# Kernel tuning notes

Measured on AMD Instinct MI355X. Metric: run time of the kernel, lower is better.

## Reference

```python
import jax, jax.numpy as jnp
import numpy as np

B, N, K = 4, 4096, 20
IN_C, OUT_C = 32, 32
EPS = 1e-5


def setup_inputs() -> dict:
    key = jax.random.key(0)
    ks = jax.random.split(key, 10)
    s = 0.05
    return {
        "x": jax.random.normal(ks[0], (B, 3, N), dtype=jnp.float32),
        "feature": jax.random.normal(ks[1], (B, IN_C, N), dtype=jnp.float32),
        "w_mlp": jax.random.normal(ks[2], (IN_C, 7), dtype=jnp.float32) * s,     # Conv1d(7, in_c, 1)
        "b_mlp": jax.random.normal(ks[3], (IN_C,), dtype=jnp.float32) * s,
        "w_att": jax.random.normal(ks[4], (2 * IN_C, 2 * IN_C), dtype=jnp.float32) * s,  # Conv1d(2C,2C,1,bias=False)
        "w_conv": jax.random.normal(ks[5], (OUT_C, 2 * IN_C), dtype=jnp.float32) * s,    # Linear(2C,out_c)
        "b_conv": jax.random.normal(ks[6], (OUT_C,), dtype=jnp.float32) * s,
        "w_out": jax.random.normal(ks[7], (OUT_C, IN_C), dtype=jnp.float32) * s,  # Conv1d(in_c,out_c,1)
        "b_out": jax.random.normal(ks[8], (OUT_C,), dtype=jnp.float32) * s,
        "gamma": jnp.ones((OUT_C,), dtype=jnp.float32),   # BatchNorm1d weight
        "beta": jnp.zeros((OUT_C,), dtype=jnp.float32),   # BatchNorm1d bias
    }


def reference(x, feature, w_mlp, b_mlp, w_att, w_conv, b_conv, w_out, b_out, gamma, beta):
    pts = jnp.swapaxes(x, 1, 2)                       # [B, N, 3]
    # brute-force KNN (argkmin over squared distance); self is nearest (d=0)
    sq = jnp.sum(pts * pts, axis=-1)                  # [B, N]
    d2 = sq[:, :, None] + sq[:, None, :] - 2.0 * jnp.einsum('bnd,bmd->bnm', pts, pts)
    neigh = jax.lax.top_k(-d2, K)[1]                  # [B, N, K] int32

    gather = jax.vmap(lambda v, idx: v[idx])          # per-batch fancy gather
    x_neighs = gather(pts, neigh)                     # [B, N, K, 3]
    x_repeat = jnp.broadcast_to(x_neighs[:, :, 0:1, :], x_neighs.shape)
    x_rel = x_neighs - x_repeat                       # [B, N, K, 3]
    x_dis = jnp.linalg.norm(x_rel, axis=-1, keepdims=True)  # [B, N, K, 1]
    x_feats = jnp.concatenate([x_repeat, x_rel, x_dis], axis=-1)   # [B, N, K, 7]
    x_enc = jnp.einsum('bnkf,cf->bnkc', x_feats, w_mlp) + b_mlp    # [B, N, K, C]

    feat_pts = jnp.swapaxes(feature, 1, 2)            # [B, N, C]
    feat_neighs = gather(feat_pts, neigh)             # [B, N, K, C]
    feats = jnp.concatenate([feat_neighs, x_enc], axis=-1)         # [B, N, K, 2C]

    # attention weights: pointwise conv then softmax over the CHANNEL dim (torch dim=1)
    scores = jnp.einsum('bnkc,dc->bnkd', feats, w_att)             # [B, N, K, 2C]
    attn = jax.nn.softmax(scores, axis=-1)
    pooled = jnp.sum(attn * feats, axis=2)            # sum over neighbors K -> [B, N, 2C]

    out_feat = jnp.einsum('bnc,oc->bno', pooled, w_conv) + b_conv  # [B, N, out_c]
    out_feat = jnp.swapaxes(out_feat, 1, 2)           # [B, out_c, N]
    out_feat = out_feat + jnp.einsum('oc,bcn->bon', w_out, feature) + b_out[None, :, None]

    # BatchNorm1d (training-mode batch statistics over B and N)
    mean = jnp.mean(out_feat, axis=(0, 2), keepdims=True)
    var = jnp.var(out_feat, axis=(0, 2), keepdims=True)
    normed = (out_feat - mean) * jax.lax.rsqrt(var + EPS)
    return normed * gamma[None, :, None] + beta[None, :, None]
```

## Files before the change

### kernel.cpp

```cpp
#include <hip/hip_runtime.h>
#include <hip/hip_bf16.h>

#define BATCH 4
#define NPTS  4096
#define KNBR  20
#define INC   32
#define TWC   64
#define OUTC  32
#define EPSBN 1e-5f

typedef short short8 __attribute__((ext_vector_type(8)));
typedef float f32x16 __attribute__((ext_vector_type(16)));

__device__ __forceinline__ float rlf(float v, int l) {
    return __uint_as_float((unsigned)__builtin_amdgcn_readlane((int)__float_as_uint(v), l));
}
__device__ __forceinline__ ushort f2bf(float x) {
    unsigned u = __float_as_uint(x);
    unsigned r = u + 0x7FFFu + ((u >> 16) & 1u);
    return (ushort)(r >> 16);
}
__device__ __forceinline__ float bf2f(ushort h) {
    return __uint_as_float(((unsigned)h) << 16);
}
__device__ __forceinline__ void gll16(const float4* g, float4* l) {
    __builtin_amdgcn_global_load_lds((const __attribute__((address_space(1))) void*)g,
                                     (__attribute__((address_space(3))) void*)l, 16, 0, 0);
}

__global__ __launch_bounds__(256) void k_prep(const float* __restrict__ x,
                                              const float* __restrict__ f,
                                              float4* __restrict__ xT4,
                                              ushort* __restrict__ fT,
                                              const float* __restrict__ w_att,
                                              const float* __restrict__ w_conv,
                                              const float* __restrict__ w_out,
                                              const float* __restrict__ w_mlp,
                                              const float* __restrict__ b_mlp,
                                              short8* __restrict__ wattF,
                                              short8* __restrict__ wconvF,
                                              short8* __restrict__ woutF,
                                              float* __restrict__ wmlp8) {
    int i = blockIdx.x * 256 + threadIdx.x;
    if (i < BATCH * NPTS) {
        int b = i / NPTS, n = i % NPTS;
        const float* xb = x + (size_t)b * 3 * NPTS;
        float x0 = xb[n], x1 = xb[NPTS + n], x2 = xb[2 * NPTS + n];
        float sq = fmaf(x2, x2, fmaf(x1, x1, x0 * x0));
        xT4[i] = make_float4(x0, x1, x2, sq);
    }
    if (i < BATCH * INC * NPTS) {
        int n = i % NPTS; int t = i / NPTS; int c = t % INC; int b = t / INC;
        fT[((size_t)(b * NPTS + n)) * INC + c] = f2bf(f[i]);
    }
    if (blockIdx.x == gridDim.x - 1) {
        int t = threadIdx.x;
        for (int idx = t; idx < 14 * 64; idx += 256) {
            int fr = idx >> 6, ln = idx & 63, l31 = ln & 31, h8 = (ln >> 5) * 8;
            short8 v;
            if (fr < 8) {
                int nt = fr >> 2, kt = fr & 3;
                const float* s = w_att + (nt * 32 + l31) * 64 + kt * 16 + h8;
#pragma unroll
                for (int j = 0; j < 8; ++j) v[j] = (short)f2bf(s[j]);
                wattF[fr * 64 + ln] = v;
            } else if (fr < 12) {
                int kt = fr - 8;
                const float* s = w_conv + l31 * 64 + kt * 16 + h8;
#pragma unroll
                for (int j = 0; j < 8; ++j) v[j] = (short)f2bf(s[j]);
                wconvF[kt * 64 + ln] = v;
            } else {
                int kt = fr - 12;
                const float* s = w_out + l31 * 32 + kt * 16 + h8;
#pragma unroll
                for (int j = 0; j < 8; ++j) v[j] = (short)f2bf(s[j]);
                woutF[kt * 64 + ln] = v;
            }
        }
        for (int idx = t; idx < 512; idx += 256) {
            int e = idx >> 3, j = idx & 7;
            wmlp8[idx] = (j < 7) ? w_mlp[e * 7 + j] : b_mlp[e];
        }
    }
}

#define CAP   192
#define PPBK  8
#define FWSZ  (KNBR * 64)
__global__ __launch_bounds__(512, 6) void k_fused(const float4* __restrict__ xT4,
                                                  const ushort* __restrict__ fbT,
                                                  const float* __restrict__ wmlp8,
                                                  const short8* __restrict__ wattF,
                                                  const short8* __restrict__ wconvF,
                                                  const short8* __restrict__ woutF,
                                                  float* __restrict__ out) {
    __shared__ __align__(16) char smA[28672];
    float4*             candB = (float4*)smA;
    unsigned long long* survB = (unsigned long long*)(smA + 16384);
    ushort*             FbB   = (ushort*)smA;
    __shared__ int scnt[PPBK], slot[PPBK];
    __shared__ int neighL[PPBK][KNBR];
    __shared__ __align__(16) ushort pool[PPBK][64];

    const int tid  = threadIdx.x;
    const int lane = tid & 63;
    const int wv   = tid >> 6;
    const int hi   = lane >> 5;
    const int l31  = lane & 31;
    const int gp   = blockIdx.x * PPBK + wv;
    const int b    = gp >> 12;
    const int nb   = gp & (NPTS - 1);
    const float4* base = xT4 + (size_t)b * NPTS;

    if (lane == 0) { scnt[wv] = 0; slot[wv] = 1; }

    float4 me = xT4[gp];

    auto stage = [&](int c) {
        const float4* src = base + c * 512 + wv * 64 + lane;
        float4* dst = candB + (c & 1) * 512 + wv * 64;
        gll16(src, dst);
    };

    stage(0); stage(1);
    __syncthreads();

    unsigned bits[16];
    unsigned lmin = 0xFFFFFFFFu, lmin2 = 0xFFFFFFFFu;
#pragma unroll
    for (int j = 0; j < 8; ++j) {
        float4 o = candB[lane + 64 * j];
        float dot = fmaf(o.z, me.z, fmaf(o.y, me.y, o.x * me.x));
        unsigned bb = __float_as_uint(fmaxf((me.w + o.w) - 2.0f * dot, 0.0f));
        bits[j] = bb;
        unsigned lo_ = bb < lmin ? bb : lmin;
        unsigned hi_ = bb < lmin ? lmin : bb;
        lmin = lo_;
        lmin2 = hi_ < lmin2 ? hi_ : lmin2;
    }
#pragma unroll
    for (int j = 0; j < 8; ++j) {
        float4 o = candB[512 + lane + 64 * j];
        float dot = fmaf(o.z, me.z, fmaf(o.y, me.y, o.x * me.x));
        unsigned bb = __float_as_uint(fmaxf((me.w + o.w) - 2.0f * dot, 0.0f));
        bits[8 + j] = bb;
        unsigned lo_ = bb < lmin ? bb : lmin;
        unsigned hi_ = bb < lmin ? lmin : bb;
        lmin = lo_;
        lmin2 = hi_ < lmin2 ? hi_ : lmin2;
    }
    __syncthreads();
    stage(2);

    unsigned lo = 0u, hi2 = 0xFF000000u;
    for (int it = 0; it < 16 && lo < hi2; ++it) {
        unsigned mid = lo + ((hi2 - lo) >> 1);
        int c = __popcll(__ballot(lmin <= mid)) + __popcll(__ballot(lmin2 <= mid));
        if (c >= KNBR) hi2 = mid; else lo = mid + 1;
    }
    const unsigned tau = hi2;

#pragma unroll
    for (int j = 0; j < 16; ++j) {
        if (bits[j] <= tau) {
            int pos = atomicAdd(&scnt[wv], 1);
            if (pos < CAP)
                survB[wv * CAP + pos] = ((unsigned long long)bits[j] << 32) | (unsigned)(lane + 64 * j);
        }
    }
    __syncthreads();

    for (int ch = 2; ch < 8; ++ch) {
        if (ch < 7) stage(ch + 1);
        const float4* cb = candB + (ch & 1) * 512;
        const int ib = ch * 512 + lane;
#pragma unroll
        for (int j = 0; j < 8; ++j) {
            float4 o = cb[lane + 64 * j];
            float dot = fmaf(o.z, me.z, fmaf(o.y, me.y, o.x * me.x));
            unsigned bb = __float_as_uint(fmaxf((me.w + o.w) - 2.0f * dot, 0.0f));
            if (bb <= tau) {
                int pos = atomicAdd(&scnt[wv], 1);
                if (pos < CAP)
                    survB[wv * CAP + pos] = ((unsigned long long)bb << 32) | (unsigned)(ib + 64 * j);
            }
        }
        __syncthreads();
    }

    int cnt = scnt[wv]; if (cnt > CAP) cnt = CAP;
    const unsigned long long* sv = survB + wv * CAP;

    if (cnt <= 128) {
        unsigned long long k0 = (lane      < cnt) ? sv[lane     ] : ~0ull;
        unsigned long long k1 = (lane + 64 < cnt) ? sv[lane + 64] : ~0ull;
        unsigned d0 = (unsigned)(k0 >> 32), d1 = (unsigned)(k1 >> 32);
        unsigned i0 = (unsigned)k0, i1 = (unsigned)k1;

        unsigned th;
        {
            unsigned l2 = 0u, h2 = tau;
            bool found = false;
            for (int it = 0; it < 32; ++it) {
                unsigned mid = l2 + ((h2 - l2) >> 1);
                int c = __popcll(__ballot(d0 <= mid)) + __popcll(__ballot(d1 <= mid));
                if (c >= KNBR) h2 = mid; else l2 = mid + 1;
                if (c == KNBR) {
                    unsigned mm = (d0 <= mid) ? d0 : 0u;
                    unsigned m2_ = (d1 <= mid) ? d1 : 0u;
                    mm = mm > m2_ ? mm : m2_;
#pragma unroll
                    for (int off = 32; off >= 1; off >>= 1) {
                        unsigned o = __shfl_xor(mm, off, 64);
                        mm = o > mm ? o : mm;
                    }
                    th = mm; found = true; break;
                }
                if (l2 >= h2) break;
            }
            if (!found) th = h2;
        }
        int cless = __popcll(__ballot(d0 < th)) + __popcll(__ballot(d1 < th));
        int need = KNBR - cless;
        bool t0 = (d0 == th), t1 = (d1 == th);
        int tcnt = __popcll(__ballot(t0)) + __popcll(__ballot(t1));
        unsigned idxthr = 0xFFFFFFFFu;
        if (tcnt != need) {
            unsigned la = 0u, ha = 0xFFFFFFFFu;
            for (int it = 0; it < 32; ++it) {
                unsigned mid = la + ((ha - la) >> 1);
                int c = __popcll(__ballot(t0 && i0 <= mid)) + __popcll(__ballot(t1 && i1 <= mid));
                if (c >= need) ha = mid; else la = mid + 1;
            }
            idxthr = ha;
        }
        bool s0 = (d0 < th) || (t0 && i0 <= idxthr);
        bool s1 = (d1 < th) || (t1 && i1 <= idxthr);

        unsigned long long mk = k0 < k1 ? k0 : k1;
#pragma unroll
        for (int off = 32; off >= 1; off >>= 1) {
            unsigned long long o = __shfl_xor(mk, off, 64);
            mk = o < mk ? o : mk;
        }
        if (s0) { if (k0 == mk) neighL[wv][0] = (int)i0; else { int p = atomicAdd(&slot[wv], 1); neighL[wv][p] = (int)i0; } }
        if (s1) { if (k1 == mk) neighL[wv][0] = (int)i1; else { int p = atomicAdd(&slot[wv], 1); neighL[wv][p] = (int)i1; } }
    } else {
        unsigned long long k0 = (lane       < cnt) ? sv[lane      ] : ~0ull;
        unsigned long long k1 = (lane +  64 < cnt) ? sv[lane +  64] : ~0ull;
        unsigned long long k2 = (lane + 128 < cnt) ? sv[lane + 128] : ~0ull;
        unsigned d0 = (unsigned)(k0 >> 32), d1 = (unsigned)(k1 >> 32), d2 = (unsigned)(k2 >> 32);
        unsigned i0 = (unsigned)k0, i1 = (unsigned)k1, i2 = (unsigned)k2;

        unsigned l2 = 0u, h2 = tau;
        for (int it = 0; it < 32 && l2 < h2; ++it) {
            unsigned mid = l2 + ((h2 - l2) >> 1);
            int c = __popcll(__ballot(d0 <= mid)) + __popcll(__ballot(d1 <= mid))
                  + __popcll(__ballot(d2 <= mid));
            if (c >= KNBR) h2 = mid; else l2 = mid + 1;
        }
        const unsigned th = h2;
        int cless = __popcll(__ballot(d0 < th)) + __popcll(__ballot(d1 < th))
                  + __popcll(__ballot(d2 < th));
        int need = KNBR - cless;
        bool t0 = (d0 == th), t1 = (d1 == th), t2 = (d2 == th);
        int tcnt = __popcll(__ballot(t0)) + __popcll(__ballot(t1)) + __popcll(__ballot(t2));
        unsigned idxthr = 0xFFFFFFFFu;
        if (tcnt != need) {
            unsigned la = 0u, ha = 0xFFFFFFFFu;
            for (int it = 0; it < 32; ++it) {
                unsigned mid = la + ((ha - la) >> 1);
                int c = __popcll(__ballot(t0 && i0 <= mid)) + __popcll(__ballot(t1 && i1 <= mid))
                      + __popcll(__ballot(t2 && i2 <= mid));
                if (c >= need) ha = mid; else la = mid + 1;
            }
            idxthr = ha;
        }
        bool s0 = (d0 < th) || (t0 && i0 <= idxthr);
        bool s1 = (d1 < th) || (t1 && i1 <= idxthr);
        bool s2 = (d2 < th) || (t2 && i2 <= idxthr);

        unsigned long long m01 = k0 < k1 ? k0 : k1;
        unsigned long long mk  = m01 < k2 ? m01 : k2;
#pragma unroll
        for (int off = 32; off >= 1; off >>= 1) {
            unsigned long long o = __shfl_xor(mk, off, 64);
            mk = o < mk ? o : mk;
        }
        if (s0) { if (k0 == mk) neighL[wv][0] = (int)i0; else { int p = atomicAdd(&slot[wv], 1); neighL[wv][p] = (int)i0; } }
        if (s1) { if (k1 == mk) neighL[wv][0] = (int)i1; else { int p = atomicAdd(&slot[wv], 1); neighL[wv][p] = (int)i1; } }
        if (s2) { if (k2 == mk) neighL[wv][0] = (int)i2; else { int p = atomicAdd(&slot[wv], 1); neighL[wv][p] = (int)i2; } }
    }

    __syncthreads();

    const ushort* fb = fbT + (size_t)b * NPTS * INC;
    ushort* Fw = FbB + wv * FWSZ;

    int nv = 0;
    if (l31 < KNBR) nv = neighL[wv][l31];
    float4 ncl = base[nv];

    float wm[8];
    {
        const float4* w8 = (const float4*)(wmlp8 + l31 * 8);
        float4 a = w8[0], bq = w8[1];
        wm[0] = a.x; wm[1] = a.y; wm[2] = a.z; wm[3] = a.w;
        wm[4] = bq.x; wm[5] = bq.y; wm[6] = bq.z; wm[7] = bq.w;
    }
    const float c0x = rlf(ncl.x, 0), c0y = rlf(ncl.y, 0), c0z = rlf(ncl.z, 0);

    ushort fr[KNBR];
#pragma unroll
    for (int k = 0; k < KNBR; ++k) {
        int snk = __builtin_amdgcn_readlane(nv, k);
        fr[k] = fb[(size_t)snk * INC + l31];
    }

    float rxl = ncl.x - c0x, ryl = ncl.y - c0y, rzl = ncl.z - c0z;
    float disl = sqrtf(fmaf(rzl, rzl, fmaf(ryl, ryl, rxl * rxl)));

    float fmbase = wm[7];
    fmbase = fmaf(wm[0], c0x, fmbase); fmbase = fmaf(wm[1], c0y, fmbase);
    fmbase = fmaf(wm[2], c0z, fmbase);
#pragma unroll
    for (int k = 0; k < KNBR; ++k) {
        float fm = fmbase;
        fm = fmaf(wm[3], rlf(rxl, k), fm);
        fm = fmaf(wm[4], rlf(ryl, k), fm);
        fm = fmaf(wm[5], rlf(rzl, k), fm);
        fm = fmaf(wm[6], rlf(disl, k), fm);
        ushort fbits = hi ? f2bf(fm) : fr[k];
        Fw[k * 64 + (lane ^ ((k & 7) << 3))] = fbits;
    }

    const int rowA = (l31 < KNBR) ? l31 : (KNBR - 1);
    short8 Af[4];
#pragma unroll
    for (int kt = 0; kt < 4; ++kt) {
        int c0 = kt * 16 + 8 * hi;
        Af[kt] = *(const short8*)&Fw[rowA * 64 + (c0 ^ ((rowA & 7) << 3))];
    }

    float mloc, zloc;
    {
        f32x16 af;
#pragma unroll
        for (int i = 0; i < 16; ++i) af[i] = 0.f;
        __builtin_amdgcn_s_setprio(1);
#pragma unroll
        for (int kt = 0; kt < 4; ++kt)
            af = __builtin_amdgcn_mfma_f32_32x32x16_bf16(wattF[kt * 64 + lane], Af[kt], af, 0, 0, 0);
        __builtin_amdgcn_s_setprio(0);
        float m0 = af[0];
#pragma unroll
        for (int i = 1; i < 16; ++i) m0 = fmaxf(m0, af[i]);
        float z0 = 0.f;
#pragma unroll
        for (int i = 0; i < 16; ++i) z0 += __expf(af[i] - m0);
        mloc = m0; zloc = z0;
    }
    {
        f32x16 af;
#pragma unroll
        for (int i = 0; i < 16; ++i) af[i] = 0.f;
        __builtin_amdgcn_s_setprio(1);
#pragma unroll
        for (int kt = 0; kt < 4; ++kt)
            af = __builtin_amdgcn_mfma_f32_32x32x16_bf16(wattF[(4 + kt) * 64 + lane], Af[kt], af, 0, 0, 0);
        __builtin_amdgcn_s_setprio(0);
        float m1 = af[0];
#pragma unroll
        for (int i = 1; i < 16; ++i) m1 = fmaxf(m1, af[i]);
        float z1 = 0.f;
#pragma unroll
        for (int i = 0; i < 16; ++i) z1 += __expf(af[i] - m1);
        float mn = fmaxf(mloc, m1);
        zloc = zloc * __expf(mloc - mn) + z1 * __expf(m1 - mn);
        mloc = mn;
    }
    float mo = fmaxf(mloc, __shfl_xor(mloc, 32, 64));
    float zs = zloc * __expf(mloc - mo);
    float Zk = zs + __shfl_xor(zs, 32, 64);
    float mzl = mo + __logf(Zk);

    float pooled0 = 0.f, pooled1 = 0.f;
    {
        f32x16 acc;
#pragma unroll
        for (int i = 0; i < 16; ++i) acc[i] = 0.f;
        __builtin_amdgcn_s_setprio(1);
#pragma unroll
        for (int kt = 0; kt < 4; ++kt)
            acc = __builtin_amdgcn_mfma_f32_32x32x16_bf16(Af[kt], wattF[kt * 64 + lane], acc, 0, 0, 0);
        __builtin_amdgcn_s_setprio(0);
#pragma unroll
        for (int r = 0; r < 12; ++r) {
            int j = (r & 3) + 8 * (r >> 2) + 4 * hi;
            float a0 = __expf(acc[r] - rlf(mzl, j));
            float f0 = bf2f(Fw[j * 64 + (l31 ^ ((j & 7) << 3))]);
            float p0 = a0 * f0;
            if (r >= 8) p0 = hi ? 0.f : p0;
            pooled0 += p0;
        }
    }
    {
        f32x16 acc;
#pragma unroll
        for (int i = 0; i < 16; ++i) acc[i] = 0.f;
        __builtin_amdgcn_s_setprio(1);
#pragma unroll
        for (int kt = 0; kt < 4; ++kt)
            acc = __builtin_amdgcn_mfma_f32_32x32x16_bf16(Af[kt], wattF[(4 + kt) * 64 + lane], acc, 0, 0, 0);
        __builtin_amdgcn_s_setprio(0);
#pragma unroll
        for (int r = 0; r < 12; ++r) {
            int j = (r & 3) + 8 * (r >> 2) + 4 * hi;
            float a1 = __expf(acc[r] - rlf(mzl, j));
            float f1 = bf2f(Fw[j * 64 + ((32 + l31) ^ ((j & 7) << 3))]);
            float p1 = a1 * f1;
            if (r >= 8) p1 = hi ? 0.f : p1;
            pooled1 += p1;
        }
    }
    pooled0 += __shfl_xor(pooled0, 32, 64);
    pooled1 += __shfl_xor(pooled1, 32, 64);
    if (!hi) {
        pool[wv][l31]      = f2bf(pooled0);
        pool[wv][32 + l31] = f2bf(pooled1);
    }

    f32x16 oa;
#pragma unroll
    for (int i = 0; i < 16; ++i) oa[i] = 0.f;
    __builtin_amdgcn_s_setprio(1);
#pragma unroll
    for (int kt = 0; kt < 4; ++kt) {
        short8 bb = *(const short8*)&pool[wv][kt * 16 + 8 * hi];
        oa = __builtin_amdgcn_mfma_f32_32x32x16_bf16(wconvF[kt * 64 + lane], bb, oa, 0, 0, 0);
    }
#pragma unroll
    for (int kt = 0; kt < 2; ++kt) {
        short8 bb = *(const short8*)(fb + (size_t)nb * INC + kt * 16 + 8 * hi);
        oa = __builtin_amdgcn_mfma_f32_32x32x16_bf16(woutF[kt * 64 + lane], bb, oa, 0, 0, 0);
    }
    __builtin_amdgcn_s_setprio(0);
#pragma unroll
    for (int r = 0; r < 16; ++r) {
        int o = (r & 3) + 8 * (r >> 2) + 4 * hi;
        if (l31 == 0) out[((size_t)(b * OUTC + o)) * NPTS + nb] = oa[r];
    }
}

__global__ __launch_bounds__(256) void k_bn(float* __restrict__ of,
                                            const float* __restrict__ gamma,
                                            const float* __restrict__ beta) {
    const int c = blockIdx.x;
    const int tid = threadIdx.x;
    float s = 0.f, s2 = 0.f;
#pragma unroll
    for (int b = 0; b < BATCH; ++b) {
        const float4* p = (const float4*)(of + ((size_t)b * OUTC + c) * NPTS);
        for (int i = tid; i < NPTS / 4; i += 256) {
            float4 v = p[i];
            s += (v.x + v.y) + (v.z + v.w);
            s2 = fmaf(v.x, v.x, s2); s2 = fmaf(v.y, v.y, s2);
            s2 = fmaf(v.z, v.z, s2); s2 = fmaf(v.w, v.w, s2);
        }
    }
#pragma unroll
    for (int off = 32; off >= 1; off >>= 1) {
        s += __shfl_xor(s, off, 64);
        s2 += __shfl_xor(s2, off, 64);
    }
    __shared__ float rs[4], rs2[4];
    __shared__ float sc[2];
    if ((tid & 63) == 0) { rs[tid >> 6] = s; rs2[tid >> 6] = s2; }
    __syncthreads();
    if (tid == 0) {
        float S = (rs[0] + rs[1]) + (rs[2] + rs[3]);
        float S2 = (rs2[0] + rs2[1]) + (rs2[2] + rs2[3]);
        const float invn = 1.0f / (BATCH * NPTS);
        float mean = S * invn;
        float var = S2 * invn - mean * mean;
        float rstd = rsqrtf(var + EPSBN);
        float scale = rstd * gamma[c];
        sc[0] = scale;
        sc[1] = beta[c] - mean * scale;
    }
    __syncthreads();
    const float scale = sc[0], shift = sc[1];
#pragma unroll
    for (int b = 0; b < BATCH; ++b) {
        float4* p = (float4*)(of + ((size_t)b * OUTC + c) * NPTS);
        for (int i = tid; i < NPTS / 4; i += 256) {
            float4 v = p[i];
            v.x = fmaf(v.x, scale, shift);
            v.y = fmaf(v.y, scale, shift);
            v.z = fmaf(v.z, scale, shift);
            v.w = fmaf(v.w, scale, shift);
            p[i] = v;
        }
    }
}

extern "C" void kernel_launch(void* const* d_in, const int* in_sizes, int n_in,
                              void* d_out, int out_size, void* d_ws, size_t ws_size,
                              hipStream_t stream) {
    const float* x      = (const float*)d_in[0];
    const float* feat   = (const float*)d_in[1];
    const float* w_mlp  = (const float*)d_in[2];
    const float* b_mlp  = (const float*)d_in[3];
    const float* w_att  = (const float*)d_in[4];
    const float* w_conv = (const float*)d_in[5];
    const float* w_out  = (const float*)d_in[7];
    const float* gamma  = (const float*)d_in[9];
    const float* beta   = (const float*)d_in[10];
    float* out = (float*)d_out;

    char* ws = (char*)d_ws;
    float4* xT4    = (float4*)ws;
    ushort* fbT    = (ushort*)(ws + 262144);
    short8* wattF  = (short8*)(ws + 1310976);
    short8* wconvF = (short8*)(ws + 1319168);
    short8* woutF  = (short8*)(ws + 1323264);
    float*  wmlp8  = (float*)(ws + 1325312);

    k_prep<<<(BATCH * INC * NPTS + 255) / 256 + 1, 256, 0, stream>>>(
        x, feat, xT4, fbT, w_att, w_conv, w_out, w_mlp, b_mlp,
        wattF, wconvF, woutF, wmlp8);
    k_fused<<<(BATCH * NPTS) / PPBK, 512, 0, stream>>>(xT4, fbT, wmlp8,
                                                       wattF, wconvF, woutF, out);
    k_bn<<<OUTC, 256, 0, stream>>>(out, gamma, beta);
}
```

Baseline: 84.92 us.

## Triple-buffer KNN candidate staging with explicit vmcnt waits and raw barriers

Measured after the change: 84.49 us, median of 2. Within noise of the previous version (-0.5%).

```diff
diff --git a/kernel.cpp b/kernel.cpp
--- a/kernel.cpp
+++ b/kernel.cpp
@@ -26,6 +26,16 @@
 __device__ __forceinline__ void gll16(const float4* g, float4* l) {
     __builtin_amdgcn_global_load_lds((const __attribute__((address_space(1))) void*)g,
                                      (__attribute__((address_space(3))) void*)l, 16, 0, 0);
+}
+__device__ __forceinline__ void barrier_nd() {
+    asm volatile("" ::: "memory");
+    __builtin_amdgcn_s_barrier();
+    asm volatile("" ::: "memory");
+}
+template <int N> __device__ __forceinline__ void waitVm() {
+    if constexpr (N == 0) asm volatile("s_waitcnt vmcnt(0)" ::: "memory");
+    else if constexpr (N == 1) asm volatile("s_waitcnt vmcnt(1)" ::: "memory");
+    else asm volatile("s_waitcnt vmcnt(2)" ::: "memory");
 }
 
 __global__ __launch_bounds__(256) void k_prep(const float* __restrict__ x,
@@ -95,9 +105,9 @@
                                                   const short8* __restrict__ wconvF,
                                                   const short8* __restrict__ woutF,
                                                   float* __restrict__ out) {
-    __shared__ __align__(16) char smA[28672];
+    __shared__ __align__(16) char smA[36864];
     float4*             candB = (float4*)smA;
-    unsigned long long* survB = (unsigned long long*)(smA + 16384);
+    unsigned long long* survB = (unsigned long long*)(smA + 24576);
     ushort*             FbB   = (ushort*)smA;
     __shared__ int scnt[PPBK], slot[PPBK];
     __shared__ int neighL[PPBK][KNBR];
@@ -116,42 +126,46 @@
     if (lane == 0) { scnt[wv] = 0; slot[wv] = 1; }
 
     float4 me = xT4[gp];
+    asm volatile("s_waitcnt vmcnt(0)" ::: "memory");
 
     auto stage = [&](int c) {
         const float4* src = base + c * 512 + wv * 64 + lane;
-        float4* dst = candB + (c & 1) * 512 + wv * 64;
+        float4* dst = candB + (c % 3) * 512 + wv * 64;
         gll16(src, dst);
     };
-
-    stage(0); stage(1);
-    __syncthreads();
+    auto dist = [&](const float4& o) -> unsigned {
+        float dot = fmaf(o.z, me.z, fmaf(o.y, me.y, o.x * me.x));
+        return __float_as_uint(fmaxf((me.w + o.w) - 2.0f * dot, 0.0f));
+    };
+
+    stage(0); stage(1); stage(2);
 
     unsigned bits[16];
     unsigned lmin = 0xFFFFFFFFu, lmin2 = 0xFFFFFFFFu;
+
+    waitVm<2>(); barrier_nd();
 #pragma unroll
     for (int j = 0; j < 8; ++j) {
-        float4 o = candB[lane + 64 * j];
-        float dot = fmaf(o.z, me.z, fmaf(o.y, me.y, o.x * me.x));
-        unsigned bb = __float_as_uint(fmaxf((me.w + o.w) - 2.0f * dot, 0.0f));
+        unsigned bb = dist(candB[lane + 64 * j]);
         bits[j] = bb;
         unsigned lo_ = bb < lmin ? bb : lmin;
         unsigned hi_ = bb < lmin ? lmin : bb;
         lmin = lo_;
         lmin2 = hi_ < lmin2 ? hi_ : lmin2;
     }
+    barrier_nd(); stage(3);
+
+    waitVm<2>(); barrier_nd();
 #pragma unroll
     for (int j = 0; j < 8; ++j) {
-        float4 o = candB[512 + lane + 64 * j];
-        float dot = fmaf(o.z, me.z, fmaf(o.y, me.y, o.x * me.x));
-        unsigned bb = __float_as_uint(fmaxf((me.w + o.w) - 2.0f * dot, 0.0f));
+        unsigned bb = dist(candB[512 + lane + 64 * j]);
         bits[8 + j] = bb;
         unsigned lo_ = bb < lmin ? bb : lmin;
         unsigned hi_ = bb < lmin ? lmin : bb;
         lmin = lo_;
         lmin2 = hi_ < lmin2 ? hi_ : lmin2;
     }
-    __syncthreads();
-    stage(2);
+    barrier_nd(); stage(4);
 
     unsigned lo = 0u, hi2 = 0xFF000000u;
     for (int it = 0; it < 16 && lo < hi2; ++it) {
@@ -169,24 +183,24 @@
                 survB[wv * CAP + pos] = ((unsigned long long)bits[j] << 32) | (unsigned)(lane + 64 * j);
         }
     }
-    __syncthreads();
-
+
+#pragma unroll
     for (int ch = 2; ch < 8; ++ch) {
-        if (ch < 7) stage(ch + 1);
-        const float4* cb = candB + (ch & 1) * 512;
+        if (ch <= 5) waitVm<2>(); else if (ch == 6) waitVm<1>(); else waitVm<0>();
+        barrier_nd();
+        const float4* cb = candB + (ch % 3) * 512;
         const int ib = ch * 512 + lane;
 #pragma unroll
         for (int j = 0; j < 8; ++j) {
-            float4 o = cb[lane + 64 * j];
-            float dot = fmaf(o.z, me.z, fmaf(o.y, me.y, o.x * me.x));
-            unsigned bb = __float_as_uint(fmaxf((me.w + o.w) - 2.0f * dot, 0.0f));
+            unsigned bb = dist(cb[lane + 64 * j]);
             if (bb <= tau) {
                 int pos = atomicAdd(&scnt[wv], 1);
                 if (pos < CAP)
                     survB[wv * CAP + pos] = ((unsigned long long)bb << 32) | (unsigned)(ib + 64 * j);
             }
         }
-        __syncthreads();
+        barrier_nd();
+        if (ch < 5) stage(ch + 3);
     }
 
     int cnt = scnt[wv]; if (cnt > CAP) cnt = CAP;
```
